# Performance work log

Measured on AMD Instinct MI355X. Metric: run time of the kernel, lower is better.

The kernel has to match this reference:

```python
import jax, jax.numpy as jnp
import numpy as np
import math

B, A, S, H = 4, 3, 1024, 768
NH, HD = 12, 64  # num_heads, head_dim
TEMP = 1.0
LN_EPS = 1e-5


def setup_inputs() -> dict:
    key = jax.random.key(0)
    ks = jax.random.split(key, 8)
    w_scale = math.sqrt(6.0 / (H + H))  # xavier_uniform
    def lin_w(k):
        return jax.random.uniform(k, (H, H), jnp.float32, -w_scale, w_scale)
    return {
        "query": jax.random.normal(ks[0], (B, S, H), jnp.float32),
        "adapter_outputs": jax.random.normal(ks[1], (B, A, S, H), jnp.float32),
        "Wq": lin_w(ks[2]), "bq": jnp.zeros((H,), jnp.float32),
        "Wk": lin_w(ks[3]), "bk": jnp.zeros((H,), jnp.float32),
        "Wv": lin_w(ks[4]), "bv": jnp.zeros((H,), jnp.float32),
        "Wo": lin_w(ks[5]), "bo": jnp.zeros((H,), jnp.float32),
        "gamma": jnp.ones((H,), jnp.float32),
        "beta": jnp.zeros((H,), jnp.float32),
    }


def reference(query, adapter_outputs, Wq, bq, Wk, bk, Wv, bv, Wo, bo, gamma, beta):
    # Q: [B,S,H] -> [B,NH,S,HD]
    Q = (query @ Wq.T + bq).reshape(B, S, NH, HD).transpose(0, 2, 1, 3)
    # K,V: [B,A,S,H] -> [B,NH,A,S,HD] (vectorizes the per-adapter torch loop)
    K = (adapter_outputs @ Wk.T + bk).reshape(B, A, S, NH, HD).transpose(0, 3, 1, 2, 4)
    V = (adapter_outputs @ Wv.T + bv).reshape(B, A, S, NH, HD).transpose(0, 3, 1, 2, 4)
    scores = jnp.einsum('bhqd,bhasd->bhqas', Q, K) / (math.sqrt(HD) * TEMP)
    # softmax over the ADAPTER axis only (dim=3), as in the original
    attn = jax.nn.softmax(scores, axis=3)
    # sum over both adapters and source positions
    attended = jnp.einsum('bhqas,bhasd->bhqd', attn, V)
    attended = attended.transpose(0, 2, 1, 3).reshape(B, S, H)
    out = attended @ Wo.T + bo
    x = out + query
    mu = jnp.mean(x, axis=-1, keepdims=True)
    var = jnp.mean(jnp.square(x - mu), axis=-1, keepdims=True)
    out = (x - mu) * jax.lax.rsqrt(var + LN_EPS) * gamma + beta
    avg_weights = attn.mean(axis=1).mean(axis=2)  # [B,Q,S]
    return out, avg_weights
```

## Files before the change

### kernel.cpp

```cpp
#include <hip/hip_runtime.h>

#define NB 4
#define NA 3
#define NS 1024
#define NHID 768
#define NHEADS 12
#define HD 64

typedef __bf16 bf16_t;
typedef __bf16 bf16x8 __attribute__((ext_vector_type(8)));
typedef __bf16 bf16x4 __attribute__((ext_vector_type(4)));
typedef float f32x4 __attribute__((ext_vector_type(4)));

#define MFMA(a, b, c) __builtin_amdgcn_mfma_f32_16x16x32_bf16(a, b, c, 0, 0, 0)

static __device__ __forceinline__ bf16x8 load8(const bf16_t* p) {
    return *reinterpret_cast<const bf16x8*>(p);
}

typedef __attribute__((address_space(3))) unsigned int u32_lds;
typedef __attribute__((address_space(1))) unsigned int u32_glb;
static __device__ __forceinline__ void gl_lds16(const void* g, void* lds_base_uniform) {
    __builtin_amdgcn_global_load_lds((const u32_glb*)g, (u32_lds*)lds_base_uniform, 16, 0, 0);
}

static __device__ __forceinline__ bf16x8 cvt8(f32x4 lo, f32x4 hi) {
    bf16x8 r;
    r[0] = (bf16_t)lo[0]; r[1] = (bf16_t)lo[1]; r[2] = (bf16_t)lo[2]; r[3] = (bf16_t)lo[3];
    r[4] = (bf16_t)hi[0]; r[5] = (bf16_t)hi[1]; r[6] = (bf16_t)hi[2]; r[7] = (bf16_t)hi[3];
    return r;
}


__global__ __launch_bounds__(256) void cvt6(
    const float* __restrict__ s0, bf16_t* __restrict__ d0, int c0,
    const float* __restrict__ s1, bf16_t* __restrict__ d1, int c1,
    const float* __restrict__ s2, bf16_t* __restrict__ d2, int c2,
    const float* __restrict__ s3, bf16_t* __restrict__ d3, int c3,
    const float* __restrict__ s4, bf16_t* __restrict__ d4, int c4,
    const float* __restrict__ s5, bf16_t* __restrict__ d5, int c5)
{
    const int bid = blockIdx.x;
    const float* s; bf16_t* d; int rel;
    if      (bid < c0) { s = s0; d = d0; rel = bid; }
    else if (bid < c1) { s = s1; d = d1; rel = bid - c0; }
    else if (bid < c2) { s = s2; d = d2; rel = bid - c1; }
    else if (bid < c3) { s = s3; d = d3; rel = bid - c2; }
    else if (bid < c4) { s = s4; d = d4; rel = bid - c3; }
    else               { s = s5; d = d5; rel = bid - c4; }
    const int t = threadIdx.x;
#pragma unroll
    for (int k = 0; k < 4; k++) {
        size_t u = (size_t)rel * 1024 + k * 256 + t;
        f32x4 v = reinterpret_cast<const f32x4*>(s)[u];
        bf16x4 o;
        o[0] = (bf16_t)v[0]; o[1] = (bf16_t)v[1];
        o[2] = (bf16_t)v[2]; o[3] = (bf16_t)v[3];
        reinterpret_cast<bf16x4*>(d)[u] = o;
    }
}

__global__ __launch_bounds__(512) void gemm8(
    const bf16_t* __restrict__ X,
    const bf16_t* __restrict__ W0, const bf16_t* __restrict__ W1,
    const float* __restrict__ bias0, const float* __restrict__ bias1,
    bf16_t* __restrict__ outK, bf16_t* __restrict__ outV,
    const bf16_t* __restrict__ X2, const bf16_t* __restrict__ W2,
    const float* __restrict__ bias2, bf16_t* __restrict__ outQ)
{
    constexpr int BUFSZ = 49152;
    __shared__ __align__(16) char smem[3 * BUFSZ];

    const int t = threadIdx.x;
    const int lane = t & 63, w = t >> 6;
    const int quad = lane >> 4, l15 = lane & 15;
    const int wm = w >> 1, wn = w & 1;

    int emode = 1, nt = 12, bid = blockIdx.x;
    const bf16_t* Xp = X;
    const bf16_t* Wp = W0;
    const float*  b0 = bias0;
    if (bid >= 576) {
        emode = 0; nt = 6; bid -= 576;
        Xp = X2; Wp = W2; b0 = bias2;
    }

    const int xcd = bid & 7, jj = bid >> 3;
    const int n_t = jj % nt, slab = jj / nt;
    const int m0 = (slab * 8 + xcd) * 256;
    const int n0 = n_t * 128;

    const bf16_t* Wsel = (emode == 1 && n0 >= 768) ? W1 : Wp;
    const int n0b = (emode == 1 && n0 >= 768) ? n0 - 768 : n0;

    const bf16_t* sp[6];
    int loff[6];
#pragma unroll
    for (int i = 0; i < 6; i++) {
        int g = w * 6 + i;
        loff[i] = g * 1024;
        if (g < 32) {
            int ks = g >> 4, mt = g & 15;
            sp[i] = Xp + (size_t)(m0 + mt * 16 + l15) * NHID + ks * 32 + quad * 8;
        } else {
            int gb = g - 32;
            int ks = gb >> 3, ntile = gb & 7;
            sp[i] = Wsel + (size_t)(n0b + ntile * 16 + l15) * NHID + ks * 32 + quad * 8;
        }
    }

    auto stage_half = [&](char* base, int h) {
#pragma unroll
        for (int i = 0; i < 3; i++) {
            int idx = h * 3 + i;
            gl_lds16(sp[idx], base + loff[idx]);
            sp[idx] += 64;
        }
    };

    f32x4 acc[4][4];
#pragma unroll
    for (int i = 0; i < 4; i++)
#pragma unroll
        for (int j = 0; j < 4; j++) acc[i][j] = 0.0f;

    constexpr int KITER = NHID / 64;
    stage_half(smem, 0);          stage_half(smem, 1);
    stage_half(smem + BUFSZ, 0);  stage_half(smem + BUFSZ, 1);

    for (int it = 0; it < KITER; ++it) {
        if (it == KITER - 1) asm volatile("s_waitcnt vmcnt(0)" ::: "memory");
        else                 asm volatile("s_waitcnt vmcnt(6)" ::: "memory");
        __builtin_amdgcn_s_barrier();

        const char* rb = smem + (it % 3) * BUFSZ;
        char* pb = smem + ((it + 2) % 3) * BUFSZ;
        const bool dostage = (it + 2 < KITER);

#pragma unroll
        for (int ks = 0; ks < 2; ++ks) {
            bf16x8 af[4], bfr[4];
#pragma unroll
            for (int i = 0; i < 4; i++)
                af[i] = *(const bf16x8*)(rb + (ks * 16 + wm * 4 + i) * 1024 + lane * 16);
#pragma unroll
            for (int j = 0; j < 4; j++)
                bfr[j] = *(const bf16x8*)(rb + 32768 + (ks * 8 + wn * 4 + j) * 1024 + lane * 16);
            if (dostage) stage_half(pb, ks);
            __builtin_amdgcn_s_setprio(1);
#pragma unroll
            for (int i = 0; i < 4; i++)
#pragma unroll
                for (int j = 0; j < 4; j++)
                    acc[i][j] = MFMA(af[i], bfr[j], acc[i][j]);
            __builtin_amdgcn_s_setprio(0);
            if (ks == 0) __builtin_amdgcn_s_barrier();
        }
    }

#pragma unroll
    for (int i = 0; i < 4; i++) {
#pragma unroll
        for (int j = 0; j < 4; j++) {
            const int n = n0 + wn * 64 + j * 16 + l15;
            float bn;
            if (emode == 1) bn = (n < 768) ? b0[n] : bias1[n - 768];
            else            bn = b0[n];
            if (emode == 1 && n >= 768) {
                const int m = m0 + wm * 64 + i * 16 + quad * 4;
                int b = m / (NA * NS);
                int rem = m - b * (NA * NS);
                int a = rem >> 10, s = rem & 1023;
                int hh = (n - 768) >> 6;
                bf16x4 pk;
#pragma unroll
                for (int rg = 0; rg < 4; rg++) pk[rg] = (bf16_t)(acc[i][j][rg] + bn);
                char* dst = (char*)outV + (size_t)((b * NHEADS + hh) * NA + a) * 131072
                            + (size_t)(s >> 5) * 4096 + j * 1024
                            + (quad * 16 + l15) * 16 + (i & 1) * 8;
                *reinterpret_cast<bf16x4*>(dst) = pk;
            } else {
#pragma unroll
                for (int rg = 0; rg < 4; rg++) {
                    const int m = m0 + wm * 64 + i * 16 + quad * 4 + rg;
                    float v = acc[i][j][rg] + bn;
                    if (emode == 0) {
                        int b = m >> 10, s = m & 1023, hh = n >> 6, d = n & 63;
                        outQ[(((size_t)(b * NHEADS + hh) * NS) + s) * HD + d] = (bf16_t)v;
                    } else {
                        int b = m / (NA * NS);
                        int rem = m - b * (NA * NS);
                        int a = rem >> 10, s = rem & 1023;
                        int hh = n >> 6, d = n & 63;
                        outK[((((size_t)(b * NHEADS + hh) * NA + a) * NS) + s) * HD + d] = (bf16_t)v;
                    }
                }
            }
        }
    }
}

template <int MODE, int NT, bool ABF, bool BBF>
__global__ __launch_bounds__(256) void proj_gemm(
    const void* __restrict__ Xv,
    const void* __restrict__ W0v, const void* __restrict__ W1v,
    const float* __restrict__ bias0, const float* __restrict__ bias1,
    const float* __restrict__ resid,
    bf16_t* __restrict__ out0, bf16_t* __restrict__ out1,
    float* __restrict__ outf)
{
    constexpr int ASZ   = ABF ? 8192 : 16384;
    constexpr int BSZ   = BBF ? 8192 : 16384;
    constexpr int BUFSZ = ASZ + BSZ;
    constexpr int LPS   = (ABF ? 2 : 4) + (BBF ? 2 : 4);
    __shared__ __align__(16) char smem[2 * BUFSZ];

    const int t = threadIdx.x;
    const int lane = t & 63, w = t >> 6;
    const int quad = lane >> 4, l15 = lane & 15;
    const int wm = w >> 1, wn = w & 1;

    const int bid = blockIdx.x;
    const int xcd = bid & 7, jj = bid >> 3;
    const int n_t = jj % NT, slab = jj / NT;
    const int m0 = (slab * 8 + xcd) * 128;
    const int n0 = n_t * 128;

    const void* Wselv = (MODE == 1 && n0 >= 768) ? W1v : W0v;
    const int n0b = (MODE == 1 && n0 >= 768) ? n0 - 768 : n0;

    const int srow  = lane >> 3;
    const int schnk = (lane & 7) ^ srow;
    const float*  Apf[4];
    const bf16_t* Apb[2];
    const float*  Bpf[4];
    const bf16_t* Bpb[2];
    if constexpr (ABF) {
        const bf16_t* X = (const bf16_t*)Xv;
#pragma unroll
        for (int i = 0; i < 2; i++) {
            int g = w * 2 + i;
            Apb[i] = X + (size_t)(m0 + g * 16 + l15) * NHID + quad * 8;
        }
    } else {
        const float* X = (const float*)Xv;
#pragma unroll
        for (int i = 0; i < 4; i++) {
            int g = w * 4 + i;
            Apf[i] = X + (size_t)(m0 + g * 8 + srow) * NHID + schnk * 4;
        }
    }
    if constexpr (BBF) {
        const bf16_t* Wb = (const bf16_t*)Wselv;
#pragma unroll
        for (int i = 0; i < 2; i++) {
            int g = w * 2 + i;
            Bpb[i] = Wb + (size_t)(n0b + g * 16 + l15) * NHID + quad * 8;
        }
    } else {
        const float* Wf = (const float*)Wselv;
#pragma unroll
        for (int i = 0; i < 4; i++) {
            int g = w * 4 + i;
            Bpf[i] = Wf + (size_t)(n0b + g * 8 + srow) * NHID + schnk * 4;
        }
    }

    auto stage = [&](char* base) {
        char* Ab = base;
        char* Bb = base + ASZ;
        if constexpr (ABF) {
#pragma unroll
            for (int i = 0; i < 2; i++) { gl_lds16(Apb[i], Ab + (w * 2 + i) * 1024); Apb[i] += 32; }
        } else {
#pragma unroll
            for (int i = 0; i < 4; i++) { gl_lds16(Apf[i], Ab + (w * 4 + i) * 1024); Apf[i] += 32; }
        }
        if constexpr (BBF) {
#pragma unroll
            for (int i = 0; i < 2; i++) { gl_lds16(Bpb[i], Bb + (w * 2 + i) * 1024); Bpb[i] += 32; }
        } else {
#pragma unroll
            for (int i = 0; i < 4; i++) { gl_lds16(Bpf[i], Bb + (w * 4 + i) * 1024); Bpf[i] += 32; }
        }
    };

    auto wait_one = [&]() {
        if constexpr (LPS == 4)      asm volatile("s_waitcnt vmcnt(4)" ::: "memory");
        else if constexpr (LPS == 6) asm volatile("s_waitcnt vmcnt(6)" ::: "memory");
        else                         asm volatile("s_waitcnt vmcnt(8)" ::: "memory");
    };

    f32x4 acc[4][4];
#pragma unroll
    for (int i = 0; i < 4; i++)
#pragma unroll
        for (int j = 0; j < 4; j++) acc[i][j] = 0.0f;

    constexpr int KITER = NHID / 32;
    stage(smem);

    for (int it = 0; it < KITER; ++it) {
        if (it + 1 < KITER) {
            stage(smem + ((it + 1) & 1) * BUFSZ);
            wait_one();
        } else {
            asm volatile("s_waitcnt vmcnt(0)" ::: "memory");
        }
        __builtin_amdgcn_s_barrier();

        char* Ab = smem + (it & 1) * BUFSZ;
        char* Bb = Ab + ASZ;

        bf16x8 af[4], bfr[4];
        const int pl = (2 * quad) ^ (l15 & 7);
#pragma unroll
        for (int i = 0; i < 4; i++) {
            if constexpr (ABF) {
                int mt = wm * 4 + i;
                af[i] = *(const bf16x8*)(Ab + (mt * 64 + lane) * 16);
            } else {
                int R = (wm * 4 + i) * 16 + l15;
                f32x4 lo = *(const f32x4*)(Ab + R * 128 + pl * 16);
                f32x4 hi = *(const f32x4*)(Ab + R * 128 + (pl ^ 1) * 16);
                af[i] = cvt8(lo, hi);
            }
        }
#pragma unroll
        for (int j = 0; j < 4; j++) {
            if constexpr (BBF) {
                int ntj = wn * 4 + j;
                bfr[j] = *(const bf16x8*)(Bb + (ntj * 64 + lane) * 16);
            } else {
                int R = (wn * 4 + j) * 16 + l15;
                f32x4 lo = *(const f32x4*)(Bb + R * 128 + pl * 16);
                f32x4 hi = *(const f32x4*)(Bb + R * 128 + (pl ^ 1) * 16);
                bfr[j] = cvt8(lo, hi);
            }
        }
#pragma unroll
        for (int i = 0; i < 4; i++)
#pragma unroll
            for (int j = 0; j < 4; j++)
                acc[i][j] = MFMA(af[i], bfr[j], acc[i][j]);
        __builtin_amdgcn_s_barrier();
    }

#pragma unroll
    for (int i = 0; i < 4; i++) {
#pragma unroll
        for (int j = 0; j < 4; j++) {
            const int n = n0 + wn * 64 + j * 16 + l15;
            float bn;
            if (MODE == 1) bn = (n < 768) ? bias0[n] : bias1[n - 768];
            else           bn = bias0[n];
            if (MODE == 1 && n >= 768) {
                const int m = m0 + wm * 64 + i * 16 + quad * 4;
                int b = m / (NA * NS);
                int rem = m - b * (NA * NS);
                int a = rem >> 10, s = rem & 1023;
                int hh = (n - 768) >> 6;
                bf16x4 pk;
#pragma unroll
                for (int rg = 0; rg < 4; rg++) pk[rg] = (bf16_t)(acc[i][j][rg] + bn);
                char* dst = (char*)out1 + (size_t)((b * NHEADS + hh) * NA + a) * 131072
                            + (size_t)(s >> 5) * 4096 + j * 1024
                            + (quad * 16 + l15) * 16 + (i & 1) * 8;
                *reinterpret_cast<bf16x4*>(dst) = pk;
            } else {
#pragma unroll
                for (int rg = 0; rg < 4; rg++) {
                    const int m = m0 + wm * 64 + i * 16 + quad * 4 + rg;
                    float v = acc[i][j][rg] + bn;
                    if (MODE == 0) {
                        int b = m >> 10, s = m & 1023, hh = n >> 6, d = n & 63;
                        out0[(((size_t)(b * NHEADS + hh) * NS) + s) * HD + d] = (bf16_t)v;
                    } else if (MODE == 1) {
                        int b = m / (NA * NS);
                        int rem = m - b * (NA * NS);
                        int a = rem >> 10, s = rem & 1023;
                        int hh = n >> 6, d = n & 63;
                        out0[((((size_t)(b * NHEADS + hh) * NA + a) * NS) + s) * HD + d] = (bf16_t)v;
                    } else {
                        v += resid[(size_t)m * NHID + n];
                        outf[(size_t)m * NHID + n] = v;
                    }
                }
            }
        }
    }
}

__global__ __launch_bounds__(256, 3) void attn_kernel(
    const bf16_t* __restrict__ Q, const bf16_t* __restrict__ K,
    const bf16_t* __restrict__ VT, bf16_t* __restrict__ AT)
{
    __shared__ __align__(16) char kv[2 * 24576];

    const int t    = threadIdx.x;
    const int w    = t >> 6, lane = t & 63;
    const int quad = lane >> 4, l15 = lane & 15;

    int bh, qt;
    if (gridDim.x == 768) {
        int xcd = blockIdx.x & 7, j = blockIdx.x >> 3;
        bh = (j >> 4) * 8 + xcd;
        qt = ((j & 15) << 2) | w;
    } else {
        bh = blockIdx.x >> 4;
        qt = ((blockIdx.x & 15) << 2) | w;
    }
    const int b  = bh / NHEADS, h = bh - b * NHEADS;
    const int q0 = qt * 16;

    const bf16_t* Qb = Q + ((size_t)bh * NS + q0) * HD;
    bf16x8 qf0 = load8(Qb + l15 * HD + quad * 8);
    bf16x8 qf1 = load8(Qb + l15 * HD + quad * 8 + 32);

    const char* gp[6];
    int gdelta[6], loff[6];
#pragma unroll
    for (int i = 0; i < 6; i++) {
        int g = w * 6 + i;
        loff[i] = g >= 12 ? 12288 + (g - 12) * 1024 : g * 1024;
        if (g < 12) {
            int a = g >> 2, j = (g >> 1) & 1, dh = g & 1;
            gp[i] = (const char*)(K + ((size_t)(bh * NA + a) * NS + j * 16 + l15) * HD
                                  + dh * 32 + quad * 8);
            gdelta[i] = 32 * HD * 2;
        } else {
            int gi = g - 12;
            int a = gi >> 2, dt = gi & 3;
            gp[i] = (const char*)VT + (size_t)(bh * NA + a) * 131072
                    + dt * 1024 + (size_t)lane * 16;
            gdelta[i] = 4096;
        }
    }

    auto stage = [&](int buf) {
#pragma unroll
        for (int i = 0; i < 6; i++) {
            gl_lds16(gp[i], kv + buf * 24576 + loff[i]);
            gp[i] += gdelta[i];
        }
    };

    f32x4 acc[4];
#pragma unroll
    for (int dt = 0; dt < 4; dt++) acc[dt] = 0.0f;

    const float KS = 0.18033688011112042f;

    stage(0);

    for (int it = 0; it < 32; ++it) {
        if (it + 1 < 32) {
            stage((it + 1) & 1);
            asm volatile("s_waitcnt vmcnt(6)" ::: "memory");
        } else {
            asm volatile("s_waitcnt vmcnt(0)" ::: "memory");
        }
        __builtin_amdgcn_s_barrier();

        const char* base = kv + (it & 1) * 24576;
        f32x4 sc[3][2];
#pragma unroll
        for (int a = 0; a < 3; a++) {
#pragma unroll
            for (int j = 0; j < 2; j++) {
                bf16x8 klo = *(const bf16x8*)(base + ((a * 4 + j * 2 + 0) * 64 + lane) * 16);
                bf16x8 khi = *(const bf16x8*)(base + ((a * 4 + j * 2 + 1) * 64 + lane) * 16);
                f32x4 z = 0.0f;
                f32x4 c0 = MFMA(klo, qf0, z);
                sc[a][j] = MFMA(khi, qf1, c0);
            }
        }
        f32x4 plo[3], phi[3];
#pragma unroll
        for (int j = 0; j < 2; j++) {
#pragma unroll
            for (int rg = 0; rg < 4; rg++) {
                float x0 = sc[0][j][rg], x1 = sc[1][j][rg], x2 = sc[2][j][rg];
                float mx = fmaxf(x0, fmaxf(x1, x2));
                float e0 = __builtin_amdgcn_exp2f((x0 - mx) * KS);
                float e1 = __builtin_amdgcn_exp2f((x1 - mx) * KS);
                float e2 = __builtin_amdgcn_exp2f((x2 - mx) * KS);
                float inv = __builtin_amdgcn_rcpf(e0 + e1 + e2);
                if (j == 0) {
                    plo[0][rg] = e0 * inv; plo[1][rg] = e1 * inv; plo[2][rg] = e2 * inv;
                } else {
                    phi[0][rg] = e0 * inv; phi[1][rg] = e1 * inv; phi[2][rg] = e2 * inv;
                }
            }
        }
#pragma unroll
        for (int a = 0; a < 3; a++) {
            bf16x8 pf = cvt8(plo[a], phi[a]);
#pragma unroll
            for (int dt = 0; dt < 4; dt++) {
                bf16x8 vf = *(const bf16x8*)(base + 12288 + ((a * 4 + dt) * 64 + lane) * 16);
                acc[dt] = MFMA(pf, vf, acc[dt]);
            }
        }
        __builtin_amdgcn_s_barrier();
    }

    bf16_t* Ob = AT + (size_t)b * NS * NHID;
#pragma unroll
    for (int dt = 0; dt < 4; dt++) {
#pragma unroll
        for (int rg = 0; rg < 4; rg++) {
            int qq = q0 + quad * 4 + rg;
            Ob[(size_t)qq * NHID + h * HD + dt * 16 + l15] = (bf16_t)acc[dt][rg];
        }
    }
}

__global__ __launch_bounds__(256) void ln_kernel(
    float* __restrict__ X, const float* __restrict__ gamma,
    const float* __restrict__ beta)
{
    const int row = blockIdx.x;
    const int t = threadIdx.x;
    float* x = X + (size_t)row * NHID;
    float v0 = x[t], v1 = x[t + 256], v2 = x[t + 512];
    float s  = v0 + v1 + v2;
    float s2 = v0 * v0 + v1 * v1 + v2 * v2;
#pragma unroll
    for (int off = 32; off > 0; off >>= 1) {
        s  += __shfl_down(s, off);
        s2 += __shfl_down(s2, off);
    }
    __shared__ float red[8];
    const int w = t >> 6, lane = t & 63;
    if (lane == 0) { red[w] = s; red[4 + w] = s2; }
    __syncthreads();
    s  = red[0] + red[1] + red[2] + red[3];
    s2 = red[4] + red[5] + red[6] + red[7];
    float mu  = s * (1.0f / NHID);
    float var = s2 * (1.0f / NHID) - mu * mu;
    float rs  = rsqrtf(fmaxf(var, 0.0f) + 1e-5f);
    x[t]       = (v0 - mu) * rs * gamma[t]       + beta[t];
    x[t + 256] = (v1 - mu) * rs * gamma[t + 256] + beta[t + 256];
    x[t + 512] = (v2 - mu) * rs * gamma[t + 512] + beta[t + 512];
}

__global__ __launch_bounds__(256) void fill_third(float* __restrict__ p)
{
    const int i = blockIdx.x * 256 + threadIdx.x;
    f32x4 v = { 1.0f / 3.0f, 1.0f / 3.0f, 1.0f / 3.0f, 1.0f / 3.0f };
    *reinterpret_cast<f32x4*>(p + (size_t)i * 4) = v;
}

extern "C" void kernel_launch(void* const* d_in, const int* in_sizes, int n_in,
                              void* d_out, int out_size, void* d_ws, size_t ws_size,
                              hipStream_t stream)
{
    (void)in_sizes; (void)n_in; (void)out_size;
    const float* query = (const float*)d_in[0];
    const float* adapt = (const float*)d_in[1];
    const float* Wq    = (const float*)d_in[2];
    const float* bq    = (const float*)d_in[3];
    const float* Wk    = (const float*)d_in[4];
    const float* bk    = (const float*)d_in[5];
    const float* Wv    = (const float*)d_in[6];
    const float* bv    = (const float*)d_in[7];
    const float* Wo    = (const float*)d_in[8];
    const float* bo    = (const float*)d_in[9];
    const float* gamma = (const float*)d_in[10];
    const float* beta  = (const float*)d_in[11];

    float*  out0  = (float*)d_out;
    float*  out1f = out0 + 3145728;
    bf16_t* out1b = (bf16_t*)out1f;

    dim3 blk(256);

    if (ws_size >= (size_t)67633152) {
        bf16_t* Kw  = (bf16_t*)d_ws;
        bf16_t* VTw = (bf16_t*)((char*)d_ws + 18874368);
        bf16_t* Adb = (bf16_t*)((char*)d_ws + 37748736);
        bf16_t* Wqb = (bf16_t*)((char*)d_ws + 56623104);
        bf16_t* Wkb = (bf16_t*)((char*)d_ws + 57802752);
        bf16_t* Wvb = (bf16_t*)((char*)d_ws + 58982400);
        bf16_t* Wob = (bf16_t*)((char*)d_ws + 60162048);
        bf16_t* Qcb = (bf16_t*)((char*)d_ws + 61341696);
        bf16_t* Qw  = out1b;
        bf16_t* ATw = out1b + 3145728;
        cvt6<<<dim3(3648), blk, 0, stream>>>(
            adapt, Adb, 2304, query, Qcb, 3072,
            Wq, Wqb, 3216, Wk, Wkb, 3360, Wv, Wvb, 3504, Wo, Wob, 3648);
        gemm8<<<dim3(672), dim3(512), 0, stream>>>(
            Adb, Wkb, Wvb, bk, bv, Kw, VTw, Qcb, Wqb, bq, Qw);
        attn_kernel<<<dim3(768), blk, 0, stream>>>(Qw, Kw, VTw, ATw);
        proj_gemm<3, 6, true, true><<<dim3(192), blk, 0, stream>>>(
            ATw, Wob, nullptr, bo, nullptr, query, nullptr, nullptr, out0);
    } else if (ws_size >= (size_t)37748736) {
        bf16_t* Kw  = (bf16_t*)d_ws;
        bf16_t* VTw = (bf16_t*)((char*)d_ws + 18874368);
        bf16_t* Qw  = out1b;
        bf16_t* ATw = out1b + 3145728;
        bf16_t* Wqb = out1b + 6291456;
        bf16_t* Wkb = Wqb + 589824;
        bf16_t* Wvb = Wkb + 589824;
        cvt6<<<dim3(432), blk, 0, stream>>>(
            Wq, Wqb, 144, Wk, Wkb, 288, Wv, Wvb, 432,
            Wv, Wvb, 432, Wv, Wvb, 432, Wv, Wvb, 432);
        proj_gemm<0, 6, false, true><<<dim3(192), blk, 0, stream>>>(
            query, Wqb, nullptr, bq, nullptr, nullptr, Qw, nullptr, nullptr);
        proj_gemm<1, 12, false, true><<<dim3(1152), blk, 0, stream>>>(
            adapt, Wkb, Wvb, bk, bv, nullptr, Kw, VTw, nullptr);
        attn_kernel<<<dim3(768), blk, 0, stream>>>(Qw, Kw, VTw, ATw);
        proj_gemm<3, 6, true, false><<<dim3(192), blk, 0, stream>>>(
            ATw, Wo, nullptr, bo, nullptr, query, nullptr, nullptr, out0);
    } else {
        bf16_t* Qc  = out1b;
        bf16_t* ATc = out1b + 786432;
        bf16_t* Kc  = out1b + 1572864;
        bf16_t* VTc = out1b + 3932160;
        for (int b = 0; b < NB; b++) {
            const float* qb = query + (size_t)b * NS * NHID;
            const float* ab = adapt + (size_t)b * NA * NS * NHID;
            proj_gemm<0, 6, false, false><<<dim3(48), blk, 0, stream>>>(
                qb, Wq, nullptr, bq, nullptr, nullptr, Qc, nullptr, nullptr);
            proj_gemm<1, 12, false, false><<<dim3(288), blk, 0, stream>>>(
                ab, Wk, Wv, bk, bv, nullptr, Kc, VTc, nullptr);
            attn_kernel<<<dim3(192), blk, 0, stream>>>(Qc, Kc, VTc, ATc);
            proj_gemm<3, 6, true, false><<<dim3(48), blk, 0, stream>>>(
                ATc, Wo, nullptr, bo, nullptr, qb, nullptr, nullptr,
                out0 + (size_t)b * NS * NHID);
        }
    }

    ln_kernel<<<dim3(4096), blk, 0, stream>>>(out0, gamma, beta);
    fill_third<<<dim3(4096), blk, 0, stream>>>(out1f);
}
```

Before: 284.4 us.

## Process two query tiles per wave in attention and fuse fill into layernorm

The attention kernel now runs two waves per block, each handling 32 queries as two 16-row tiles. Each K and V fragment read from LDS is therefore reused across two MFMA query tiles, halving LDS read traffic per unit of compute. Each wave issues twice as many global-to-LDS copies per stage, and the block shrinks to 128 threads, which changes occupancy and latency hiding. Separately, the constant avg-weights fill is folded into the layernorm kernel to remove one launch.

```diff
diff --git a/kernel.cpp b/kernel.cpp
--- a/kernel.cpp
+++ b/kernel.cpp
@@ -391,7 +391,7 @@
     }
 }
 
-__global__ __launch_bounds__(256, 3) void attn_kernel(
+__global__ __launch_bounds__(128, 2) void attn_kernel(
     const bf16_t* __restrict__ Q, const bf16_t* __restrict__ K,
     const bf16_t* __restrict__ VT, bf16_t* __restrict__ AT)
 {
@@ -401,53 +401,55 @@
     const int w    = t >> 6, lane = t & 63;
     const int quad = lane >> 4, l15 = lane & 15;
 
-    int bh, qt;
+    int bh, qb;
     if (gridDim.x == 768) {
         int xcd = blockIdx.x & 7, j = blockIdx.x >> 3;
         bh = (j >> 4) * 8 + xcd;
-        qt = ((j & 15) << 2) | w;
+        qb = j & 15;
     } else {
         bh = blockIdx.x >> 4;
-        qt = ((blockIdx.x & 15) << 2) | w;
+        qb = blockIdx.x & 15;
     }
     const int b  = bh / NHEADS, h = bh - b * NHEADS;
-    const int q0 = qt * 16;
+    const int q0 = qb * 64 + w * 32;
 
     const bf16_t* Qb = Q + ((size_t)bh * NS + q0) * HD;
-    bf16x8 qf0 = load8(Qb + l15 * HD + quad * 8);
-    bf16x8 qf1 = load8(Qb + l15 * HD + quad * 8 + 32);
-
-    const char* gp[6];
-    int gdelta[6], loff[6];
-#pragma unroll
-    for (int i = 0; i < 6; i++) {
-        int g = w * 6 + i;
-        loff[i] = g >= 12 ? 12288 + (g - 12) * 1024 : g * 1024;
+    bf16x8 qf0[2], qf1[2];
+#pragma unroll
+    for (int t2 = 0; t2 < 2; t2++) {
+        qf0[t2] = load8(Qb + (t2 * 16 + l15) * HD + quad * 8);
+        qf1[t2] = load8(Qb + (t2 * 16 + l15) * HD + quad * 8 + 32);
+    }
+
+    const char* gp[12];
+#pragma unroll
+    for (int i = 0; i < 12; i++) {
+        int g = w * 12 + i;
         if (g < 12) {
             int a = g >> 2, j = (g >> 1) & 1, dh = g & 1;
             gp[i] = (const char*)(K + ((size_t)(bh * NA + a) * NS + j * 16 + l15) * HD
                                   + dh * 32 + quad * 8);
-            gdelta[i] = 32 * HD * 2;
         } else {
             int gi = g - 12;
             int a = gi >> 2, dt = gi & 3;
             gp[i] = (const char*)VT + (size_t)(bh * NA + a) * 131072
                     + dt * 1024 + (size_t)lane * 16;
-            gdelta[i] = 4096;
         }
     }
 
     auto stage = [&](int buf) {
 #pragma unroll
-        for (int i = 0; i < 6; i++) {
-            gl_lds16(gp[i], kv + buf * 24576 + loff[i]);
-            gp[i] += gdelta[i];
+        for (int i = 0; i < 12; i++) {
+            gl_lds16(gp[i], kv + buf * 24576 + (w * 12 + i) * 1024);
+            gp[i] += 4096;
         }
     };
 
-    f32x4 acc[4];
-#pragma unroll
-    for (int dt = 0; dt < 4; dt++) acc[dt] = 0.0f;
+    f32x4 acc[2][4];
+#pragma unroll
+    for (int t2 = 0; t2 < 2; t2++)
+#pragma unroll
+        for (int dt = 0; dt < 4; dt++) acc[t2][dt] = 0.0f;
 
     const float KS = 0.18033688011112042f;
 
@@ -456,50 +458,58 @@
     for (int it = 0; it < 32; ++it) {
         if (it + 1 < 32) {
             stage((it + 1) & 1);
-            asm volatile("s_waitcnt vmcnt(6)" ::: "memory");
+            asm volatile("s_waitcnt vmcnt(12)" ::: "memory");
         } else {
             asm volatile("s_waitcnt vmcnt(0)" ::: "memory");
         }
         __builtin_amdgcn_s_barrier();
 
         const char* base = kv + (it & 1) * 24576;
-        f32x4 sc[3][2];
+        f32x4 sc[2][3][2];
 #pragma unroll
         for (int a = 0; a < 3; a++) {
 #pragma unroll
             for (int j = 0; j < 2; j++) {
                 bf16x8 klo = *(const bf16x8*)(base + ((a * 4 + j * 2 + 0) * 64 + lane) * 16);
                 bf16x8 khi = *(const bf16x8*)(base + ((a * 4 + j * 2 + 1) * 64 + lane) * 16);
-                f32x4 z = 0.0f;
-                f32x4 c0 = MFMA(klo, qf0, z);
-                sc[a][j] = MFMA(khi, qf1, c0);
-            }
-        }
-        f32x4 plo[3], phi[3];
-#pragma unroll
-        for (int j = 0; j < 2; j++) {
-#pragma unroll
-            for (int rg = 0; rg < 4; rg++) {
-                float x0 = sc[0][j][rg], x1 = sc[1][j][rg], x2 = sc[2][j][rg];
-                float mx = fmaxf(x0, fmaxf(x1, x2));
-                float e0 = __builtin_amdgcn_exp2f((x0 - mx) * KS);
-                float e1 = __builtin_amdgcn_exp2f((x1 - mx) * KS);
-                float e2 = __builtin_amdgcn_exp2f((x2 - mx) * KS);
-                float inv = __builtin_amdgcn_rcpf(e0 + e1 + e2);
-                if (j == 0) {
-                    plo[0][rg] = e0 * inv; plo[1][rg] = e1 * inv; plo[2][rg] = e2 * inv;
-                } else {
-                    phi[0][rg] = e0 * inv; phi[1][rg] = e1 * inv; phi[2][rg] = e2 * inv;
+#pragma unroll
+                for (int t2 = 0; t2 < 2; t2++) {
+                    f32x4 z = 0.0f;
+                    f32x4 c0 = MFMA(klo, qf0[t2], z);
+                    sc[t2][a][j] = MFMA(khi, qf1[t2], c0);
                 }
             }
         }
+        f32x4 plo[2][3], phi[2][3];
+#pragma unroll
+        for (int t2 = 0; t2 < 2; t2++) {
+#pragma unroll
+            for (int j = 0; j < 2; j++) {
+#pragma unroll
+                for (int rg = 0; rg < 4; rg++) {
+                    float x0 = sc[t2][0][j][rg], x1 = sc[t2][1][j][rg], x2 = sc[t2][2][j][rg];
+                    float mx = fmaxf(x0, fmaxf(x1, x2));
+                    float e0 = __builtin_amdgcn_exp2f((x0 - mx) * KS);
+                    float e1 = __builtin_amdgcn_exp2f((x1 - mx) * KS);
+                    float e2 = __builtin_amdgcn_exp2f((x2 - mx) * KS);
+                    float inv = __builtin_amdgcn_rcpf(e0 + e1 + e2);
+                    if (j == 0) {
+                        plo[t2][0][rg] = e0 * inv; plo[t2][1][rg] = e1 * inv; plo[t2][2][rg] = e2 * inv;
+                    } else {
+                        phi[t2][0][rg] = e0 * inv; phi[t2][1][rg] = e1 * inv; phi[t2][2][rg] = e2 * inv;
+                    }
+                }
+            }
+        }
 #pragma unroll
         for (int a = 0; a < 3; a++) {
-            bf16x8 pf = cvt8(plo[a], phi[a]);
+            bf16x8 pf0 = cvt8(plo[0][a], phi[0][a]);
+            bf16x8 pf1 = cvt8(plo[1][a], phi[1][a]);
 #pragma unroll
             for (int dt = 0; dt < 4; dt++) {
                 bf16x8 vf = *(const bf16x8*)(base + 12288 + ((a * 4 + dt) * 64 + lane) * 16);
-                acc[dt] = MFMA(pf, vf, acc[dt]);
+                acc[0][dt] = MFMA(pf0, vf, acc[0][dt]);
+                acc[1][dt] = MFMA(pf1, vf, acc[1][dt]);
             }
         }
         __builtin_amdgcn_s_barrier();
@@ -507,18 +517,21 @@
 
     bf16_t* Ob = AT + (size_t)b * NS * NHID;
 #pragma unroll
-    for (int dt = 0; dt < 4; dt++) {
-#pragma unroll
-        for (int rg = 0; rg < 4; rg++) {
-            int qq = q0 + quad * 4 + rg;
-            Ob[(size_t)qq * NHID + h * HD + dt * 16 + l15] = (bf16_t)acc[dt][rg];
+    for (int t2 = 0; t2 < 2; t2++) {
+#pragma unroll
+        for (int dt = 0; dt < 4; dt++) {
+#pragma unroll
+            for (int rg = 0; rg < 4; rg++) {
+                int qq = q0 + t2 * 16 + quad * 4 + rg;
+                Ob[(size_t)qq * NHID + h * HD + dt * 16 + l15] = (bf16_t)acc[t2][dt][rg];
+            }
         }
     }
 }
 
 __global__ __launch_bounds__(256) void ln_kernel(
     float* __restrict__ X, const float* __restrict__ gamma,
-    const float* __restrict__ beta)
+    const float* __restrict__ beta, float* __restrict__ avgw)
 {
     const int row = blockIdx.x;
     const int t = threadIdx.x;
@@ -543,13 +556,8 @@
     x[t]       = (v0 - mu) * rs * gamma[t]       + beta[t];
     x[t + 256] = (v1 - mu) * rs * gamma[t + 256] + beta[t + 256];
     x[t + 512] = (v2 - mu) * rs * gamma[t + 512] + beta[t + 512];
-}
-
-__global__ __launch_bounds__(256) void fill_third(float* __restrict__ p)
-{
-    const int i = blockIdx.x * 256 + threadIdx.x;
-    f32x4 v = { 1.0f / 3.0f, 1.0f / 3.0f, 1.0f / 3.0f, 1.0f / 3.0f };
-    *reinterpret_cast<f32x4*>(p + (size_t)i * 4) = v;
+    f32x4 v3 = { 1.0f / 3.0f, 1.0f / 3.0f, 1.0f / 3.0f, 1.0f / 3.0f };
+    reinterpret_cast<f32x4*>(avgw)[(size_t)row * 256 + t] = v3;
 }
 
 extern "C" void kernel_launch(void* const* d_in, const int* in_sizes, int n_in,
@@ -575,6 +583,7 @@
     bf16_t* out1b = (bf16_t*)out1f;
 
     dim3 blk(256);
+    dim3 ablk(128);
 
     if (ws_size >= (size_t)67633152) {
         bf16_t* Kw  = (bf16_t*)d_ws;
@@ -592,7 +601,7 @@
             Wq, Wqb, 3216, Wk, Wkb, 3360, Wv, Wvb, 3504, Wo, Wob, 3648);
         gemm8<<<dim3(672), dim3(512), 0, stream>>>(
             Adb, Wkb, Wvb, bk, bv, Kw, VTw, Qcb, Wqb, bq, Qw);
-        attn_kernel<<<dim3(768), blk, 0, stream>>>(Qw, Kw, VTw, ATw);
+        attn_kernel<<<dim3(768), ablk, 0, stream>>>(Qw, Kw, VTw, ATw);
         proj_gemm<3, 6, true, true><<<dim3(192), blk, 0, stream>>>(
             ATw, Wob, nullptr, bo, nullptr, query, nullptr, nullptr, out0);
     } else if (ws_size >= (size_t)37748736) {
@@ -610,7 +619,7 @@
             query, Wqb, nullptr, bq, nullptr, nullptr, Qw, nullptr, nullptr);
         proj_gemm<1, 12, false, true><<<dim3(1152), blk, 0, stream>>>(
             adapt, Wkb, Wvb, bk, bv, nullptr, Kw, VTw, nullptr);
-        attn_kernel<<<dim3(768), blk, 0, stream>>>(Qw, Kw, VTw, ATw);
+        attn_kernel<<<dim3(768), ablk, 0, stream>>>(Qw, Kw, VTw, ATw);
         proj_gemm<3, 6, true, false><<<dim3(192), blk, 0, stream>>>(
             ATw, Wo, nullptr, bo, nullptr, query, nullptr, nullptr, out0);
     } else {
@@ -625,13 +634,12 @@
                 qb, Wq, nullptr, bq, nullptr, nullptr, Qc, nullptr, nullptr);
             proj_gemm<1, 12, false, false><<<dim3(288), blk, 0, stream>>>(
                 ab, Wk, Wv, bk, bv, nullptr, Kc, VTc, nullptr);
-            attn_kernel<<<dim3(192), blk, 0, stream>>>(Qc, Kc, VTc, ATc);
+            attn_kernel<<<dim3(192), ablk, 0, stream>>>(Qc, Kc, VTc, ATc);
             proj_gemm<3, 6, true, false><<<dim3(48), blk, 0, stream>>>(
                 ATc, Wo, nullptr, bo, nullptr, qb, nullptr, nullptr,
                 out0 + (size_t)b * NS * NHID);
         }
     }
 
-    ln_kernel<<<dim3(4096), blk, 0, stream>>>(out0, gamma, beta);
-    fill_third<<<dim3(4096), blk, 0, stream>>>(out1f);
-}
+    ln_kernel<<<dim3(4096), blk, 0, stream>>>(out0, gamma, beta, out1f);
+}
```

New measurement: 298.7 us. 5.0% more time.
